# Performance work log

Measured on AMD Instinct MI355X. Metric: run time of the kernel, lower is better.

The kernel has to match this reference:

```python
import jax, jax.numpy as jnp
import numpy as np

N, E, F, H, C = 50000, 800000, 128, 128, 64
NEG_SLOPE = 0.2


def setup_inputs() -> dict:
    key = jax.random.key(0)
    ks = jax.random.split(key, 12)
    s = 1.0 / np.sqrt(H)
    return {
        "x": jax.random.normal(ks[0], (N, F), jnp.float32),
        "edge_index": jax.random.randint(ks[1], (2, E), 0, N, jnp.int64),
        "W1": jax.random.normal(ks[2], (F, H), jnp.float32) * s,
        "b1": jnp.zeros((H,), jnp.float32),
        "Wg1": jax.random.normal(ks[3], (H, H), jnp.float32) * s,
        "asrc1": jax.random.normal(ks[4], (H,), jnp.float32) * s,
        "adst1": jax.random.normal(ks[5], (H,), jnp.float32) * s,
        "bg1": jnp.zeros((H,), jnp.float32),
        "W2": jax.random.normal(ks[6], (H, H), jnp.float32) * s,
        "b2": jnp.zeros((H,), jnp.float32),
        "Wg2": jax.random.normal(ks[7], (H, H), jnp.float32) * s,
        "asrc2": jax.random.normal(ks[8], (H,), jnp.float32) * s,
        "adst2": jax.random.normal(ks[9], (H,), jnp.float32) * s,
        "bg2": jnp.zeros((H,), jnp.float32),
        "Wo": jax.random.normal(ks[10], (H, C), jnp.float32) * s,
        "bo": jnp.zeros((C,), jnp.float32),
    }


def _gcn(x, src, dst, n, W, b):
    # PyG GCNConv: add self-loops (done by caller), symmetric normalization
    xw = x @ W
    deg = jax.ops.segment_sum(jnp.ones(src.shape[0], xw.dtype), dst, num_segments=n)
    inv = jax.lax.rsqrt(deg)  # deg >= 1 due to self-loops
    coef = inv[src] * inv[dst]
    return jax.ops.segment_sum(coef[:, None] * xw[src], dst, num_segments=n) + b


def _gat(x, src, dst, n, W, a_s, a_d, b):
    # PyG GATConv, heads=1: segment softmax over destination nodes
    xw = x @ W
    e = jax.nn.leaky_relu((xw @ a_s)[src] + (xw @ a_d)[dst], NEG_SLOPE)
    m = jax.ops.segment_max(e, dst, num_segments=n)
    ex = jnp.exp(e - m[dst])
    denom = jax.ops.segment_sum(ex, dst, num_segments=n)
    alpha = ex / denom[dst]
    return jax.ops.segment_sum(alpha[:, None] * xw[src], dst, num_segments=n) + b


def reference(x, edge_index, W1, b1, Wg1, asrc1, adst1, bg1,
              W2, b2, Wg2, asrc2, adst2, bg2, Wo, bo):
    n = x.shape[0]
    loops = jnp.arange(n, dtype=edge_index.dtype)
    src = jnp.concatenate([edge_index[0], loops])
    dst = jnp.concatenate([edge_index[1], loops])

    h = jax.nn.relu(_gcn(x, src, dst, n, W1, b1))
    h = jax.nn.relu(_gat(h, src, dst, n, Wg1, asrc1, adst1, bg1))
    h = jax.nn.relu(_gcn(h, src, dst, n, W2, b2))
    h = jax.nn.relu(_gat(h, src, dst, n, Wg2, asrc2, adst2, bg2))
    z = h @ Wo + bo
    return (h, z)
```

## Files before the change

kernel.cpp:

```cpp
#include <hip/hip_runtime.h>
#include <hip/hip_bf16.h>
#include <hip/hip_fp16.h>


#define WAVE 64
#define BK 256
#define CHUNK 4096
#define NSLICE 4

typedef _Float16 f16x8 __attribute__((ext_vector_type(8)));
typedef float f32x4 __attribute__((ext_vector_type(4)));

__global__ void k_zero_i32(int* __restrict__ p, int n) {
    int i = blockIdx.x * 256 + threadIdx.x;
    if (i < n) p[i] = 0;
}


__global__ __launch_bounds__(256) void k_bhist(
    const int* __restrict__ ei, int* __restrict__ bcnt,
    int E, int Et, int nbuck) {
    __shared__ int hist[256];
    int tid = threadIdx.x;
    if (tid < nbuck) hist[tid] = 0;
    __syncthreads();
    for (int e = blockIdx.x * 256 + tid; e < Et; e += gridDim.x * 256) {
        int d = (e < E) ? ei[E + e] : (e - E);
        atomicAdd(&hist[d >> 8], 1);
    }
    __syncthreads();
    if (tid < nbuck && hist[tid] > 0) atomicAdd(&bcnt[tid], hist[tid]);
}

__global__ void k_bscan(const int* __restrict__ bcnt, int* __restrict__ bbase,
                        int* __restrict__ bcur, int nbuck) {
    __shared__ int tmp[256];
    int tid = threadIdx.x;
    int v = (tid < nbuck) ? bcnt[tid] : 0;
    tmp[tid] = v;
    __syncthreads();
    for (int off = 1; off < 256; off <<= 1) {
        int t = (tid >= off) ? tmp[tid - off] : 0;
        __syncthreads();
        tmp[tid] += t;
        __syncthreads();
    }
    if (tid < nbuck) {
        int excl = tmp[tid] - v;
        bbase[tid] = excl;
        bcur[tid] = excl;
        if (tid == nbuck - 1) bbase[nbuck] = tmp[tid];
    }
}

__global__ __launch_bounds__(256) void k_bscatter(
    const int* __restrict__ ei, int* __restrict__ bcur,
    int2* __restrict__ ebuf, int E, int Et, int nbuck) {
    __shared__ int hist[256];
    __shared__ int base[256];
    __shared__ int off[256];
    constexpr int PT = CHUNK / 256;
    int tid = threadIdx.x;
    int cb = blockIdx.x * CHUNK;
    if (tid < nbuck) { hist[tid] = 0; off[tid] = 0; }
    __syncthreads();

    int sv[PT], dv[PT];
#pragma unroll
    for (int i = 0; i < PT; ++i) {
        int e = cb + i * 256 + tid;
        int s = 0, d = -1;
        if (e < Et) {
            if (e < E) { s = ei[e]; d = ei[E + e]; }
            else       { s = d = e - E; }
            atomicAdd(&hist[d >> 8], 1);
        }
        sv[i] = s; dv[i] = d;
    }
    __syncthreads();
    if (tid < nbuck && hist[tid] > 0)
        base[tid] = atomicAdd(&bcur[tid], hist[tid]);
    __syncthreads();
#pragma unroll
    for (int i = 0; i < PT; ++i) {
        if (dv[i] >= 0) {
            int b = dv[i] >> 8;
            int pos = base[b] + atomicAdd(&off[b], 1);
            ebuf[pos] = make_int2(sv[i], dv[i]);
        }
    }
}

__global__ __launch_bounds__(256) void k_csr(
    const int2* __restrict__ ebuf, const int* __restrict__ bbase,
    int* __restrict__ rowp, float* __restrict__ inv, int* __restrict__ esrc,
    int Nn, int Et) {
    __shared__ int hist[256];
    __shared__ int scan[256];
    __shared__ int cur[256];
    int tid = threadIdx.x;
    int b = blockIdx.x;
    int bb = bbase[b], cnt = bbase[b + 1] - bb;
    hist[tid] = 0;
    __syncthreads();
    for (int t = tid; t < cnt; t += 256)
        atomicAdd(&hist[ebuf[bb + t].y & 255], 1);
    __syncthreads();
    int v = hist[tid];
    scan[tid] = v;
    __syncthreads();
    for (int o = 1; o < 256; o <<= 1) {
        int t = (tid >= o) ? scan[tid - o] : 0;
        __syncthreads();
        scan[tid] += t;
        __syncthreads();
    }
    int excl = scan[tid] - v;
    int node = b * BK + tid;
    if (node < Nn) {
        rowp[node] = bb + excl;
        inv[node] = rsqrtf((float)v);
    }
    cur[tid] = excl;
    if (b == 0 && tid == 0) rowp[Nn] = Et;
    __syncthreads();
    for (int t = tid; t < cnt; t += 256) {
        int2 e = ebuf[bb + t];
        int pos = bb + atomicAdd(&cur[e.y & 255], 1);
        esrc[pos] = e.x;
    }
}


__global__ void k_wcvt(const float* __restrict__ W1, const float* __restrict__ Wg1,
                       const float* __restrict__ W2, const float* __restrict__ Wg2,
                       const float* __restrict__ Wo, __half* __restrict__ Wt) {
    int i = blockIdx.x * 256 + threadIdx.x;
    if (i < 65536) {
        int w = i >> 14;
        int j = i & 16383;
        int nt = j >> 11, ks = (j >> 9) & 3, lane = (j >> 3) & 63, jj = j & 7;
        int n = nt * 16 + (lane & 15);
        int k = ks * 32 + (lane >> 4) * 8 + jj;
        const float* W = (w == 0) ? W1 : (w == 1) ? Wg1 : (w == 2) ? W2 : Wg2;
        Wt[i] = __float2half(W[k * 128 + n]);
    } else if (i < 73728) {
        int j = i - 65536;
        int nt = j >> 11, ks = (j >> 9) & 3, lane = (j >> 3) & 63, jj = j & 7;
        int n = nt * 16 + (lane & 15);
        int k = ks * 32 + (lane >> 4) * 8 + jj;
        Wt[65536 + j] = __float2half(Wo[k * 64 + n]);
    }
}


template <int NC, typename OT>
__global__ __launch_bounds__(256) void gemm_mfma(
    const float* __restrict__ A, const __half* __restrict__ Wt,
    const float* __restrict__ bias, OT* __restrict__ out,
    const float* __restrict__ asrc, const float* __restrict__ adst,
    float* __restrict__ alS, float* __restrict__ alD, int M) {
    constexpr int NT = NC / 16;
    __shared__ f16x8 Wl[NC * 16];
    const int tid = threadIdx.x;
    const int wv = tid >> 6, lane = tid & 63;
    const int m16 = lane & 15, quad = lane >> 4;

#pragma unroll
    for (int i = tid; i < NC * 16; i += 256)
        Wl[i] = ((const f16x8*)Wt)[i];
    __syncthreads();

    const int row0 = blockIdx.x * 64 + wv * 16;

    f16x8 af[4];
    {
        int row = row0 + m16;
        if (row > M - 1) row = M - 1;
        const float* ap = A + (size_t)row * 128 + quad * 8;
#pragma unroll
        for (int ks = 0; ks < 4; ++ks) {
            float4 lo = *(const float4*)(ap + ks * 32);
            float4 hi = *(const float4*)(ap + ks * 32 + 4);
            f16x8 v;
            v[0] = (_Float16)lo.x; v[1] = (_Float16)lo.y;
            v[2] = (_Float16)lo.z; v[3] = (_Float16)lo.w;
            v[4] = (_Float16)hi.x; v[5] = (_Float16)hi.y;
            v[6] = (_Float16)hi.z; v[7] = (_Float16)hi.w;
            af[ks] = v;
        }
    }

    f32x4 acc[NT];
#pragma unroll
    for (int nt = 0; nt < NT; ++nt)
        acc[nt] = (f32x4){0.f, 0.f, 0.f, 0.f};

#pragma unroll
    for (int ks = 0; ks < 4; ++ks) {
#pragma unroll
        for (int nt = 0; nt < NT; ++nt) {
            f16x8 bf = Wl[(nt * 4 + ks) * 64 + lane];
            acc[nt] = __builtin_amdgcn_mfma_f32_16x16x32_f16(
                af[ks], bf, acc[nt], 0, 0, 0);
        }
    }

    if (asrc) {
        float sa[NT], da[NT];
#pragma unroll
        for (int nt = 0; nt < NT; ++nt) {
            sa[nt] = asrc[nt * 16 + m16];
            da[nt] = adst[nt * 16 + m16];
        }
#pragma unroll
        for (int r = 0; r < 4; ++r) {
            float s = 0.f, d = 0.f;
#pragma unroll
            for (int nt = 0; nt < NT; ++nt) {
                s = fmaf(acc[nt][r], sa[nt], s);
                d = fmaf(acc[nt][r], da[nt], d);
            }
#pragma unroll
            for (int off = 8; off > 0; off >>= 1) {
                s += __shfl_xor(s, off);
                d += __shfl_xor(d, off);
            }
            int row = row0 + quad * 4 + r;
            if (m16 == 0 && row < M) { alS[row] = s; alD[row] = d; }
        }
    }

#pragma unroll
    for (int nt = 0; nt < NT; ++nt) {
#pragma unroll
        for (int r = 0; r < 4; ++r) {
            int row = row0 + quad * 4 + r;
            if (row < M) {
                float v = acc[nt][r];
                int col = nt * 16 + m16;
                if constexpr (sizeof(OT) == 2) {
                    size_t addr = ((size_t)(col >> 5) * M + row) * 32 + (col & 31);
                    ((__half*)out)[addr] = __float2half(v);
                } else {
                    ((float*)out)[(size_t)row * NC + col] = v + bias[col];
                }
            }
        }
    }
}


__global__ __launch_bounds__(256) void k_wgcn(
    const int* __restrict__ rowp, const int* __restrict__ esrc,
    const float* __restrict__ inv, int2* __restrict__ ew, int Nn) {
    int gid = blockIdx.x * 256 + threadIdx.x;
    int n = gid >> 6, lane = gid & 63;
    if (n >= Nn) return;
    int beg = rowp[n], end = rowp[n + 1];
    float invd = inv[n];
    for (int e = beg + lane; e < end; e += WAVE) {
        int sid = esrc[e];
        ew[e] = make_int2(sid, __float_as_int(invd * inv[sid]));
    }
}

__global__ __launch_bounds__(256) void k_alpha(
    const int* __restrict__ rowp, const int* __restrict__ esrc,
    const float* __restrict__ as_, const float* __restrict__ ad_,
    int2* __restrict__ ew, int Nn) {
    int gid = blockIdx.x * 256 + threadIdx.x;
    int n = gid >> 6, lane = gid & 63;
    if (n >= Nn) return;
    int beg = rowp[n], end = rowp[n + 1];
    int deg = end - beg;
    float adn = ad_[n];

    if (deg <= WAVE) {
        bool valid = (lane < deg);
        int sid = 0;
        float v = -1e30f;
        if (valid) {
            sid = esrc[beg + lane];
            float t = as_[sid] + adn;
            v = (t > 0.f) ? t : 0.2f * t;
        }
        float m = v;
#pragma unroll
        for (int off = 32; off > 0; off >>= 1) m = fmaxf(m, __shfl_xor(m, off));
        float ex = valid ? __expf(v - m) : 0.f;
        float ssum = ex;
#pragma unroll
        for (int off = 32; off > 0; off >>= 1) ssum += __shfl_xor(ssum, off);
        float wgt = ex * (1.f / ssum);
        if (valid) ew[beg + lane] = make_int2(sid, __float_as_int(wgt));
    } else {
        float m = -1e30f, ssum = 0.f;
        for (int e = beg + lane; e < end; e += WAVE) {
            float v = as_[esrc[e]] + adn;
            v = (v > 0.f) ? v : 0.2f * v;
            float mn = fmaxf(m, v);
            ssum = ssum * __expf(m - mn) + __expf(v - mn);
            m = mn;
        }
#pragma unroll
        for (int off = 32; off > 0; off >>= 1) {
            float mo = __shfl_xor(m, off);
            float so = __shfl_xor(ssum, off);
            float mn = fmaxf(m, mo);
            ssum = ssum * __expf(m - mn) + so * __expf(mo - mn);
            m = mn;
        }
        float rden = 1.f / ssum;
        for (int e = beg + lane; e < end; e += WAVE) {
            int sid = esrc[e];
            float v = as_[sid] + adn;
            v = (v > 0.f) ? v : 0.2f * v;
            ew[e] = make_int2(sid, __float_as_int(__expf(v - m) * rden));
        }
    }
}


__device__ __forceinline__ void acc8(float acc[8], float4 v, float w) {
    const __half2* h2 = (const __half2*)&v;
#pragma unroll
    for (int i = 0; i < 4; ++i) {
        float2 f = __half22float2(h2[i]);
        acc[2 * i]     = fmaf(w, f.x, acc[2 * i]);
        acc[2 * i + 1] = fmaf(w, f.y, acc[2 * i + 1]);
    }
}

__global__ __launch_bounds__(256) void k_agg(
    const __half* __restrict__ xw2, const int* __restrict__ rowp,
    const int2* __restrict__ ew, const float* __restrict__ bias,
    float* __restrict__ out, int Nn) {
    int tid = threadIdx.x;
    int slice = blockIdx.x & 3;
    int nb = blockIdx.x >> 2;
    int wv = tid >> 6, lane = tid & 63;
    int n = nb * 64 + wv * 16 + (lane >> 2);
    int q = lane & 3;
    if (n >= Nn) return;
    int beg = rowp[n], end = rowp[n + 1];
    const __half* xs = xw2 + (size_t)slice * Nn * 32 + q * 8;

    float acc[8] = {0.f, 0.f, 0.f, 0.f, 0.f, 0.f, 0.f, 0.f};
    int e = beg;
    for (; e + 4 <= end; e += 4) {
        int2 p0 = ew[e], p1 = ew[e + 1], p2 = ew[e + 2], p3 = ew[e + 3];
        float4 v0 = *(const float4*)(xs + (size_t)p0.x * 32);
        float4 v1 = *(const float4*)(xs + (size_t)p1.x * 32);
        float4 v2 = *(const float4*)(xs + (size_t)p2.x * 32);
        float4 v3 = *(const float4*)(xs + (size_t)p3.x * 32);
        acc8(acc, v0, __int_as_float(p0.y));
        acc8(acc, v1, __int_as_float(p1.y));
        acc8(acc, v2, __int_as_float(p2.y));
        acc8(acc, v3, __int_as_float(p3.y));
    }
    for (; e < end; ++e) {
        int2 p = ew[e];
        float4 v = *(const float4*)(xs + (size_t)p.x * 32);
        acc8(acc, v, __int_as_float(p.y));
    }

    const float* bp = bias + slice * 32 + q * 8;
    float4 b0 = *(const float4*)(bp);
    float4 b1 = *(const float4*)(bp + 4);
    float4 r0, r1;
    r0.x = fmaxf(acc[0] + b0.x, 0.f);
    r0.y = fmaxf(acc[1] + b0.y, 0.f);
    r0.z = fmaxf(acc[2] + b0.z, 0.f);
    r0.w = fmaxf(acc[3] + b0.w, 0.f);
    r1.x = fmaxf(acc[4] + b1.x, 0.f);
    r1.y = fmaxf(acc[5] + b1.y, 0.f);
    r1.z = fmaxf(acc[6] + b1.z, 0.f);
    r1.w = fmaxf(acc[7] + b1.w, 0.f);
    float4* o = (float4*)(out + (size_t)n * 128 + slice * 32 + q * 8);
    o[0] = r0;
    o[1] = r1;
}


extern "C" void kernel_launch(void* const* d_in, const int* in_sizes, int n_in,
                              void* d_out, int out_size, void* d_ws, size_t ws_size,
                              hipStream_t stream) {
    const float* x   = (const float*)d_in[0];
    const int*   ei  = (const int*)d_in[1];
    const float* W1  = (const float*)d_in[2];
    const float* b1  = (const float*)d_in[3];
    const float* Wg1 = (const float*)d_in[4];
    const float* as1 = (const float*)d_in[5];
    const float* ad1 = (const float*)d_in[6];
    const float* bg1 = (const float*)d_in[7];
    const float* W2  = (const float*)d_in[8];
    const float* b2  = (const float*)d_in[9];
    const float* Wg2 = (const float*)d_in[10];
    const float* as2 = (const float*)d_in[11];
    const float* ad2 = (const float*)d_in[12];
    const float* bg2 = (const float*)d_in[13];
    const float* Wo  = (const float*)d_in[14];
    const float* bo  = (const float*)d_in[15];

    const int Nn = in_sizes[0] / 128;
    const int E  = in_sizes[1] / 2;
    const int Et = E + Nn;
    const int H  = 128;
    const int nbuck = (Nn + BK - 1) / BK;

    float* outH = (float*)d_out;
    float* outZ = outH + (size_t)Nn * H;

    char* p = (char*)d_ws;
    auto carve = [&](size_t bytes) {
        char* r = p;
        p += (bytes + 255) & ~(size_t)255;
        return r;
    };
    __half* bufA = (__half*)carve((size_t)Nn * H * sizeof(__half));
    __half* Wt   = (__half*)carve((size_t)73728 * sizeof(__half));
    float* alS   = (float*)carve((size_t)Nn * sizeof(float));
    float* alD   = (float*)carve((size_t)Nn * sizeof(float));
    float* inv   = (float*)carve((size_t)Nn * sizeof(float));
    int*   rowp  = (int*)carve((size_t)(Nn + 1) * sizeof(int));
    int*   esrc  = (int*)carve((size_t)Et * sizeof(int));
    int2*  ebuf  = (int2*)carve((size_t)Et * sizeof(int2));
    int2*  ewg   = (int2*)carve((size_t)Et * sizeof(int2));
    int*   bcnt  = (int*)carve((size_t)nbuck * sizeof(int));
    int*   bbase = (int*)carve((size_t)(nbuck + 1) * sizeof(int));
    int*   bcur  = (int*)carve((size_t)nbuck * sizeof(int));
    (void)ws_size; (void)n_in; (void)out_size;

    int2* ewa = ebuf;

    const int nodeWaves = (Nn * WAVE + 255) / 256;
    const int gemmB = (Nn + 63) / 64;
    const int aggB  = ((Nn + 63) / 64) * NSLICE;
    const int scatB = (Et + CHUNK - 1) / CHUNK;

    k_zero_i32<<<1, 256, 0, stream>>>(bcnt, nbuck);
    k_bhist<<<104, 256, 0, stream>>>(ei, bcnt, E, Et, nbuck);
    k_bscan<<<1, 256, 0, stream>>>(bcnt, bbase, bcur, nbuck);
    k_bscatter<<<scatB, 256, 0, stream>>>(ei, bcur, ebuf, E, Et, nbuck);
    k_csr<<<nbuck, 256, 0, stream>>>(ebuf, bbase, rowp, inv, esrc, Nn, Et);
    k_wcvt<<<288, 256, 0, stream>>>(W1, Wg1, W2, Wg2, Wo, Wt);
    k_wgcn<<<nodeWaves, 256, 0, stream>>>(rowp, esrc, inv, ewg, Nn);

    gemm_mfma<128, __half><<<gemmB, 256, 0, stream>>>(
        x, Wt, nullptr, bufA, nullptr, nullptr, nullptr, nullptr, Nn);
    k_agg<<<aggB, 256, 0, stream>>>(bufA, rowp, ewg, b1, outH, Nn);

    gemm_mfma<128, __half><<<gemmB, 256, 0, stream>>>(
        outH, Wt + 16384, nullptr, bufA, as1, ad1, alS, alD, Nn);
    k_alpha<<<nodeWaves, 256, 0, stream>>>(rowp, esrc, alS, alD, ewa, Nn);
    k_agg<<<aggB, 256, 0, stream>>>(bufA, rowp, ewa, bg1, outH, Nn);

    gemm_mfma<128, __half><<<gemmB, 256, 0, stream>>>(
        outH, Wt + 32768, nullptr, bufA, nullptr, nullptr, nullptr, nullptr, Nn);
    k_agg<<<aggB, 256, 0, stream>>>(bufA, rowp, ewg, b2, outH, Nn);

    gemm_mfma<128, __half><<<gemmB, 256, 0, stream>>>(
        outH, Wt + 49152, nullptr, bufA, as2, ad2, alS, alD, Nn);
    k_alpha<<<nodeWaves, 256, 0, stream>>>(rowp, esrc, alS, alD, ewa, Nn);
    k_agg<<<aggB, 256, 0, stream>>>(bufA, rowp, ewa, bg2, outH, Nn);

    gemm_mfma<64, float><<<gemmB, 256, 0, stream>>>(
        outH, Wt + 65536, bo, outZ, nullptr, nullptr, nullptr, nullptr, Nn);
}
```

Before: 382.0 us.

## Slice features by XCC with persistent work-stealing aggregation and fp16 intermediates

Aggregation is rewritten as a persistent kernel that splits features into 8 slices of 16 columns. Each XCC starts on its own slice and grabs node chunks through atomic cursors, so a slice's gathered rows stay in that die's cache. Intermediate hidden layers are now stored as sliced fp16 and fed straight into the next GEMM instead of fp32 rows, halving that traffic. The histogram and weight-convert kernels are merged and the zeroing kernel becomes a memset. The costs are dynamic scheduling overhead, an extra buffer, and fp16 rounding of the hidden activations.

```diff
diff --git a/kernel.cpp b/kernel.cpp
--- a/kernel.cpp
+++ b/kernel.cpp
@@ -6,20 +6,19 @@
 #define WAVE 64
 #define BK 256
 #define CHUNK 4096
-#define NSLICE 4
+#define NSL 8
+#define CURSTRIDE 16
+#define NCHUNK 128
 
 typedef _Float16 f16x8 __attribute__((ext_vector_type(8)));
 typedef float f32x4 __attribute__((ext_vector_type(4)));
 
-__global__ void k_zero_i32(int* __restrict__ p, int n) {
-    int i = blockIdx.x * 256 + threadIdx.x;
-    if (i < n) p[i] = 0;
-}
-
-
-__global__ __launch_bounds__(256) void k_bhist(
-    const int* __restrict__ ei, int* __restrict__ bcnt,
-    int E, int Et, int nbuck) {
+
+__global__ __launch_bounds__(256) void k_bhist_wcvt(
+    const int* __restrict__ ei, int* __restrict__ bcnt, int E, int Et, int nbuck,
+    const float* __restrict__ W1, const float* __restrict__ Wg1,
+    const float* __restrict__ W2, const float* __restrict__ Wg2,
+    const float* __restrict__ Wo, __half* __restrict__ Wt) {
     __shared__ int hist[256];
     int tid = threadIdx.x;
     if (tid < nbuck) hist[tid] = 0;
@@ -30,112 +29,8 @@
     }
     __syncthreads();
     if (tid < nbuck && hist[tid] > 0) atomicAdd(&bcnt[tid], hist[tid]);
-}
-
-__global__ void k_bscan(const int* __restrict__ bcnt, int* __restrict__ bbase,
-                        int* __restrict__ bcur, int nbuck) {
-    __shared__ int tmp[256];
-    int tid = threadIdx.x;
-    int v = (tid < nbuck) ? bcnt[tid] : 0;
-    tmp[tid] = v;
-    __syncthreads();
-    for (int off = 1; off < 256; off <<= 1) {
-        int t = (tid >= off) ? tmp[tid - off] : 0;
-        __syncthreads();
-        tmp[tid] += t;
-        __syncthreads();
-    }
-    if (tid < nbuck) {
-        int excl = tmp[tid] - v;
-        bbase[tid] = excl;
-        bcur[tid] = excl;
-        if (tid == nbuck - 1) bbase[nbuck] = tmp[tid];
-    }
-}
-
-__global__ __launch_bounds__(256) void k_bscatter(
-    const int* __restrict__ ei, int* __restrict__ bcur,
-    int2* __restrict__ ebuf, int E, int Et, int nbuck) {
-    __shared__ int hist[256];
-    __shared__ int base[256];
-    __shared__ int off[256];
-    constexpr int PT = CHUNK / 256;
-    int tid = threadIdx.x;
-    int cb = blockIdx.x * CHUNK;
-    if (tid < nbuck) { hist[tid] = 0; off[tid] = 0; }
-    __syncthreads();
-
-    int sv[PT], dv[PT];
-#pragma unroll
-    for (int i = 0; i < PT; ++i) {
-        int e = cb + i * 256 + tid;
-        int s = 0, d = -1;
-        if (e < Et) {
-            if (e < E) { s = ei[e]; d = ei[E + e]; }
-            else       { s = d = e - E; }
-            atomicAdd(&hist[d >> 8], 1);
-        }
-        sv[i] = s; dv[i] = d;
-    }
-    __syncthreads();
-    if (tid < nbuck && hist[tid] > 0)
-        base[tid] = atomicAdd(&bcur[tid], hist[tid]);
-    __syncthreads();
-#pragma unroll
-    for (int i = 0; i < PT; ++i) {
-        if (dv[i] >= 0) {
-            int b = dv[i] >> 8;
-            int pos = base[b] + atomicAdd(&off[b], 1);
-            ebuf[pos] = make_int2(sv[i], dv[i]);
-        }
-    }
-}
-
-__global__ __launch_bounds__(256) void k_csr(
-    const int2* __restrict__ ebuf, const int* __restrict__ bbase,
-    int* __restrict__ rowp, float* __restrict__ inv, int* __restrict__ esrc,
-    int Nn, int Et) {
-    __shared__ int hist[256];
-    __shared__ int scan[256];
-    __shared__ int cur[256];
-    int tid = threadIdx.x;
-    int b = blockIdx.x;
-    int bb = bbase[b], cnt = bbase[b + 1] - bb;
-    hist[tid] = 0;
-    __syncthreads();
-    for (int t = tid; t < cnt; t += 256)
-        atomicAdd(&hist[ebuf[bb + t].y & 255], 1);
-    __syncthreads();
-    int v = hist[tid];
-    scan[tid] = v;
-    __syncthreads();
-    for (int o = 1; o < 256; o <<= 1) {
-        int t = (tid >= o) ? scan[tid - o] : 0;
-        __syncthreads();
-        scan[tid] += t;
-        __syncthreads();
-    }
-    int excl = scan[tid] - v;
-    int node = b * BK + tid;
-    if (node < Nn) {
-        rowp[node] = bb + excl;
-        inv[node] = rsqrtf((float)v);
-    }
-    cur[tid] = excl;
-    if (b == 0 && tid == 0) rowp[Nn] = Et;
-    __syncthreads();
-    for (int t = tid; t < cnt; t += 256) {
-        int2 e = ebuf[bb + t];
-        int pos = bb + atomicAdd(&cur[e.y & 255], 1);
-        esrc[pos] = e.x;
-    }
-}
-
-
-__global__ void k_wcvt(const float* __restrict__ W1, const float* __restrict__ Wg1,
-                       const float* __restrict__ W2, const float* __restrict__ Wg2,
-                       const float* __restrict__ Wo, __half* __restrict__ Wt) {
-    int i = blockIdx.x * 256 + threadIdx.x;
+
+    int i = blockIdx.x * 256 + tid;
     if (i < 65536) {
         int w = i >> 14;
         int j = i & 16383;
@@ -153,100 +48,102 @@
     }
 }
 
-
-template <int NC, typename OT>
-__global__ __launch_bounds__(256) void gemm_mfma(
-    const float* __restrict__ A, const __half* __restrict__ Wt,
-    const float* __restrict__ bias, OT* __restrict__ out,
-    const float* __restrict__ asrc, const float* __restrict__ adst,
-    float* __restrict__ alS, float* __restrict__ alD, int M) {
-    constexpr int NT = NC / 16;
-    __shared__ f16x8 Wl[NC * 16];
-    const int tid = threadIdx.x;
-    const int wv = tid >> 6, lane = tid & 63;
-    const int m16 = lane & 15, quad = lane >> 4;
-
-#pragma unroll
-    for (int i = tid; i < NC * 16; i += 256)
-        Wl[i] = ((const f16x8*)Wt)[i];
-    __syncthreads();
-
-    const int row0 = blockIdx.x * 64 + wv * 16;
-
-    f16x8 af[4];
-    {
-        int row = row0 + m16;
-        if (row > M - 1) row = M - 1;
-        const float* ap = A + (size_t)row * 128 + quad * 8;
-#pragma unroll
-        for (int ks = 0; ks < 4; ++ks) {
-            float4 lo = *(const float4*)(ap + ks * 32);
-            float4 hi = *(const float4*)(ap + ks * 32 + 4);
-            f16x8 v;
-            v[0] = (_Float16)lo.x; v[1] = (_Float16)lo.y;
-            v[2] = (_Float16)lo.z; v[3] = (_Float16)lo.w;
-            v[4] = (_Float16)hi.x; v[5] = (_Float16)hi.y;
-            v[6] = (_Float16)hi.z; v[7] = (_Float16)hi.w;
-            af[ks] = v;
-        }
-    }
-
-    f32x4 acc[NT];
-#pragma unroll
-    for (int nt = 0; nt < NT; ++nt)
-        acc[nt] = (f32x4){0.f, 0.f, 0.f, 0.f};
-
-#pragma unroll
-    for (int ks = 0; ks < 4; ++ks) {
-#pragma unroll
-        for (int nt = 0; nt < NT; ++nt) {
-            f16x8 bf = Wl[(nt * 4 + ks) * 64 + lane];
-            acc[nt] = __builtin_amdgcn_mfma_f32_16x16x32_f16(
-                af[ks], bf, acc[nt], 0, 0, 0);
-        }
-    }
-
-    if (asrc) {
-        float sa[NT], da[NT];
-#pragma unroll
-        for (int nt = 0; nt < NT; ++nt) {
-            sa[nt] = asrc[nt * 16 + m16];
-            da[nt] = adst[nt * 16 + m16];
-        }
-#pragma unroll
-        for (int r = 0; r < 4; ++r) {
-            float s = 0.f, d = 0.f;
-#pragma unroll
-            for (int nt = 0; nt < NT; ++nt) {
-                s = fmaf(acc[nt][r], sa[nt], s);
-                d = fmaf(acc[nt][r], da[nt], d);
-            }
-#pragma unroll
-            for (int off = 8; off > 0; off >>= 1) {
-                s += __shfl_xor(s, off);
-                d += __shfl_xor(d, off);
-            }
-            int row = row0 + quad * 4 + r;
-            if (m16 == 0 && row < M) { alS[row] = s; alD[row] = d; }
-        }
-    }
-
-#pragma unroll
-    for (int nt = 0; nt < NT; ++nt) {
-#pragma unroll
-        for (int r = 0; r < 4; ++r) {
-            int row = row0 + quad * 4 + r;
-            if (row < M) {
-                float v = acc[nt][r];
-                int col = nt * 16 + m16;
-                if constexpr (sizeof(OT) == 2) {
-                    size_t addr = ((size_t)(col >> 5) * M + row) * 32 + (col & 31);
-                    ((__half*)out)[addr] = __float2half(v);
-                } else {
-                    ((float*)out)[(size_t)row * NC + col] = v + bias[col];
-                }
-            }
-        }
+__global__ void k_bscan(const int* __restrict__ bcnt, int* __restrict__ bbase,
+                        int* __restrict__ bcur, int nbuck) {
+    __shared__ int tmp[256];
+    int tid = threadIdx.x;
+    int v = (tid < nbuck) ? bcnt[tid] : 0;
+    tmp[tid] = v;
+    __syncthreads();
+    for (int off = 1; off < 256; off <<= 1) {
+        int t = (tid >= off) ? tmp[tid - off] : 0;
+        __syncthreads();
+        tmp[tid] += t;
+        __syncthreads();
+    }
+    if (tid < nbuck) {
+        int excl = tmp[tid] - v;
+        bbase[tid] = excl;
+        bcur[tid] = excl;
+        if (tid == nbuck - 1) bbase[nbuck] = tmp[tid];
+    }
+}
+
+__global__ __launch_bounds__(256) void k_bscatter(
+    const int* __restrict__ ei, int* __restrict__ bcur,
+    int2* __restrict__ ebuf, int E, int Et, int nbuck) {
+    __shared__ int hist[256];
+    __shared__ int base[256];
+    __shared__ int off[256];
+    constexpr int PT = CHUNK / 256;
+    int tid = threadIdx.x;
+    int cb = blockIdx.x * CHUNK;
+    if (tid < nbuck) { hist[tid] = 0; off[tid] = 0; }
+    __syncthreads();
+
+    int sv[PT], dv[PT];
+#pragma unroll
+    for (int i = 0; i < PT; ++i) {
+        int e = cb + i * 256 + tid;
+        int s = 0, d = -1;
+        if (e < Et) {
+            if (e < E) { s = ei[e]; d = ei[E + e]; }
+            else       { s = d = e - E; }
+            atomicAdd(&hist[d >> 8], 1);
+        }
+        sv[i] = s; dv[i] = d;
+    }
+    __syncthreads();
+    if (tid < nbuck && hist[tid] > 0)
+        base[tid] = atomicAdd(&bcur[tid], hist[tid]);
+    __syncthreads();
+#pragma unroll
+    for (int i = 0; i < PT; ++i) {
+        if (dv[i] >= 0) {
+            int b = dv[i] >> 8;
+            int pos = base[b] + atomicAdd(&off[b], 1);
+            ebuf[pos] = make_int2(sv[i], dv[i]);
+        }
+    }
+}
+
+__global__ __launch_bounds__(256) void k_csr(
+    const int2* __restrict__ ebuf, const int* __restrict__ bbase,
+    int* __restrict__ rowp, float* __restrict__ inv, int* __restrict__ esrc,
+    int Nn, int Et) {
+    __shared__ int hist[256];
+    __shared__ int scan[256];
+    __shared__ int cur[256];
+    int tid = threadIdx.x;
+    int b = blockIdx.x;
+    int bb = bbase[b], cnt = bbase[b + 1] - bb;
+    hist[tid] = 0;
+    __syncthreads();
+    for (int t = tid; t < cnt; t += 256)
+        atomicAdd(&hist[ebuf[bb + t].y & 255], 1);
+    __syncthreads();
+    int v = hist[tid];
+    scan[tid] = v;
+    __syncthreads();
+    for (int o = 1; o < 256; o <<= 1) {
+        int t = (tid >= o) ? scan[tid - o] : 0;
+        __syncthreads();
+        scan[tid] += t;
+        __syncthreads();
+    }
+    int excl = scan[tid] - v;
+    int node = b * BK + tid;
+    if (node < Nn) {
+        rowp[node] = bb + excl;
+        inv[node] = rsqrtf((float)v);
+    }
+    cur[tid] = excl;
+    if (b == 0 && tid == 0) rowp[Nn] = Et;
+    __syncthreads();
+    for (int t = tid; t < cnt; t += 256) {
+        int2 e = ebuf[bb + t];
+        int pos = bb + atomicAdd(&cur[e.y & 255], 1);
+        esrc[pos] = e.x;
     }
 }
 
@@ -322,64 +219,195 @@
 }
 
 
-__device__ __forceinline__ void acc8(float acc[8], float4 v, float w) {
-    const __half2* h2 = (const __half2*)&v;
-#pragma unroll
-    for (int i = 0; i < 4; ++i) {
-        float2 f = __half22float2(h2[i]);
-        acc[2 * i]     = fmaf(w, f.x, acc[2 * i]);
-        acc[2 * i + 1] = fmaf(w, f.y, acc[2 * i + 1]);
-    }
-}
-
-__global__ __launch_bounds__(256) void k_agg(
-    const __half* __restrict__ xw2, const int* __restrict__ rowp,
+template <typename AT, bool ASLICE, int NC, typename OT>
+__global__ __launch_bounds__(256) void gemm_mfma(
+    const AT* __restrict__ A, const __half* __restrict__ Wt,
+    const float* __restrict__ bias, OT* __restrict__ out,
+    const float* __restrict__ asrc, const float* __restrict__ adst,
+    float* __restrict__ alS, float* __restrict__ alD, int M) {
+    constexpr int NT = NC / 16;
+    __shared__ f16x8 Wl[NC * 16];
+    const int tid = threadIdx.x;
+    const int wv = tid >> 6, lane = tid & 63;
+    const int m16 = lane & 15, quad = lane >> 4;
+
+#pragma unroll
+    for (int i = tid; i < NC * 16; i += 256)
+        Wl[i] = ((const f16x8*)Wt)[i];
+    __syncthreads();
+
+    const int row0 = blockIdx.x * 64 + wv * 16;
+
+    f16x8 af[4];
+    {
+        int row = row0 + m16;
+        if (row > M - 1) row = M - 1;
+        if constexpr (ASLICE) {
+            const __half* ab = (const __half*)A;
+#pragma unroll
+            for (int ks = 0; ks < 4; ++ks) {
+                int sl = ks * 2 + (quad >> 1);
+                af[ks] = *(const f16x8*)(ab + ((size_t)sl * M + row) * 16
+                                         + (quad & 1) * 8);
+            }
+        } else {
+            const float* ap = (const float*)A + (size_t)row * 128 + quad * 8;
+#pragma unroll
+            for (int ks = 0; ks < 4; ++ks) {
+                float4 lo = *(const float4*)(ap + ks * 32);
+                float4 hi = *(const float4*)(ap + ks * 32 + 4);
+                f16x8 v;
+                v[0] = (_Float16)lo.x; v[1] = (_Float16)lo.y;
+                v[2] = (_Float16)lo.z; v[3] = (_Float16)lo.w;
+                v[4] = (_Float16)hi.x; v[5] = (_Float16)hi.y;
+                v[6] = (_Float16)hi.z; v[7] = (_Float16)hi.w;
+                af[ks] = v;
+            }
+        }
+    }
+
+    f32x4 acc[NT];
+#pragma unroll
+    for (int nt = 0; nt < NT; ++nt)
+        acc[nt] = (f32x4){0.f, 0.f, 0.f, 0.f};
+
+#pragma unroll
+    for (int ks = 0; ks < 4; ++ks) {
+#pragma unroll
+        for (int nt = 0; nt < NT; ++nt) {
+            f16x8 bf = Wl[(nt * 4 + ks) * 64 + lane];
+            acc[nt] = __builtin_amdgcn_mfma_f32_16x16x32_f16(
+                af[ks], bf, acc[nt], 0, 0, 0);
+        }
+    }
+
+    if (asrc) {
+        float sa[NT], da[NT];
+#pragma unroll
+        for (int nt = 0; nt < NT; ++nt) {
+            sa[nt] = asrc[nt * 16 + m16];
+            da[nt] = adst[nt * 16 + m16];
+        }
+#pragma unroll
+        for (int r = 0; r < 4; ++r) {
+            float s = 0.f, d = 0.f;
+#pragma unroll
+            for (int nt = 0; nt < NT; ++nt) {
+                s = fmaf(acc[nt][r], sa[nt], s);
+                d = fmaf(acc[nt][r], da[nt], d);
+            }
+#pragma unroll
+            for (int off = 8; off > 0; off >>= 1) {
+                s += __shfl_xor(s, off);
+                d += __shfl_xor(d, off);
+            }
+            int row = row0 + quad * 4 + r;
+            if (m16 == 0 && row < M) { alS[row] = s; alD[row] = d; }
+        }
+    }
+
+#pragma unroll
+    for (int nt = 0; nt < NT; ++nt) {
+#pragma unroll
+        for (int r = 0; r < 4; ++r) {
+            int row = row0 + quad * 4 + r;
+            if (row < M) {
+                float v = acc[nt][r];
+                if constexpr (sizeof(OT) == 2) {
+                    ((__half*)out)[((size_t)nt * M + row) * 16 + m16] =
+                        __float2half(v);
+                } else {
+                    int col = nt * 16 + m16;
+                    ((float*)out)[(size_t)row * NC + col] = v + bias[col];
+                }
+            }
+        }
+    }
+}
+
+
+template <typename OT>
+__global__ __launch_bounds__(256) void k_agg_slice(
+    const __half* __restrict__ xs, const int* __restrict__ rowp,
     const int2* __restrict__ ew, const float* __restrict__ bias,
-    float* __restrict__ out, int Nn) {
-    int tid = threadIdx.x;
-    int slice = blockIdx.x & 3;
-    int nb = blockIdx.x >> 2;
-    int wv = tid >> 6, lane = tid & 63;
-    int n = nb * 64 + wv * 16 + (lane >> 2);
-    int q = lane & 3;
-    if (n >= Nn) return;
-    int beg = rowp[n], end = rowp[n + 1];
-    const __half* xs = xw2 + (size_t)slice * Nn * 32 + q * 8;
-
-    float acc[8] = {0.f, 0.f, 0.f, 0.f, 0.f, 0.f, 0.f, 0.f};
-    int e = beg;
-    for (; e + 4 <= end; e += 4) {
-        int2 p0 = ew[e], p1 = ew[e + 1], p2 = ew[e + 2], p3 = ew[e + 3];
-        float4 v0 = *(const float4*)(xs + (size_t)p0.x * 32);
-        float4 v1 = *(const float4*)(xs + (size_t)p1.x * 32);
-        float4 v2 = *(const float4*)(xs + (size_t)p2.x * 32);
-        float4 v3 = *(const float4*)(xs + (size_t)p3.x * 32);
-        acc8(acc, v0, __int_as_float(p0.y));
-        acc8(acc, v1, __int_as_float(p1.y));
-        acc8(acc, v2, __int_as_float(p2.y));
-        acc8(acc, v3, __int_as_float(p3.y));
-    }
-    for (; e < end; ++e) {
-        int2 p = ew[e];
-        float4 v = *(const float4*)(xs + (size_t)p.x * 32);
-        acc8(acc, v, __int_as_float(p.y));
-    }
-
-    const float* bp = bias + slice * 32 + q * 8;
-    float4 b0 = *(const float4*)(bp);
-    float4 b1 = *(const float4*)(bp + 4);
-    float4 r0, r1;
-    r0.x = fmaxf(acc[0] + b0.x, 0.f);
-    r0.y = fmaxf(acc[1] + b0.y, 0.f);
-    r0.z = fmaxf(acc[2] + b0.z, 0.f);
-    r0.w = fmaxf(acc[3] + b0.w, 0.f);
-    r1.x = fmaxf(acc[4] + b1.x, 0.f);
-    r1.y = fmaxf(acc[5] + b1.y, 0.f);
-    r1.z = fmaxf(acc[6] + b1.z, 0.f);
-    r1.w = fmaxf(acc[7] + b1.w, 0.f);
-    float4* o = (float4*)(out + (size_t)n * 128 + slice * 32 + q * 8);
-    o[0] = r0;
-    o[1] = r1;
+    OT* __restrict__ out, int* __restrict__ cursor, int Nn) {
+    __shared__ int chunk_sh;
+    int xcc;
+    asm volatile("s_getreg_b32 %0, hwreg(HW_REG_XCC_ID)" : "=s"(xcc));
+    xcc &= 7;
+    const int tid = threadIdx.x;
+    const int wv = tid >> 6, lane = tid & 63;
+    const int j = lane >> 1, half = lane & 1;
+
+    for (int pass = 0; pass < NSL; ++pass) {
+        const int slice = (xcc + pass) & (NSL - 1);
+        int* curp = cursor + slice * CURSTRIDE;
+        const __half* xsl = xs + (size_t)slice * Nn * 16 + half * 8;
+        float b8[8];
+        *(float4*)(b8)     = *(const float4*)(bias + slice * 16 + half * 8);
+        *(float4*)(b8 + 4) = *(const float4*)(bias + slice * 16 + half * 8 + 4);
+
+        for (;;) {
+            if (tid == 0) {
+                int c = *(volatile int*)curp;
+                chunk_sh = (c >= Nn) ? Nn : atomicAdd(curp, NCHUNK);
+            }
+            __syncthreads();
+            const int n0 = chunk_sh;
+            __syncthreads();
+            if (n0 >= Nn) break;
+            const int n = n0 + wv * 32 + j;
+            if (n < Nn) {
+                int beg = rowp[n], end = rowp[n + 1];
+                float acc[8] = {0.f,0.f,0.f,0.f,0.f,0.f,0.f,0.f};
+                int e = beg;
+                for (; e + 2 <= end; e += 2) {
+                    int2 p0 = ew[e];
+                    int2 p1 = ew[e + 1];
+                    f16x8 v0 = *(const f16x8*)(xsl + (size_t)p0.x * 16);
+                    f16x8 v1 = *(const f16x8*)(xsl + (size_t)p1.x * 16);
+                    float w0 = __int_as_float(p0.y);
+                    float w1 = __int_as_float(p1.y);
+#pragma unroll
+                    for (int i = 0; i < 8; ++i)
+                        acc[i] = fmaf(w0, (float)v0[i], acc[i]);
+#pragma unroll
+                    for (int i = 0; i < 8; ++i)
+                        acc[i] = fmaf(w1, (float)v1[i], acc[i]);
+                }
+                if (e < end) {
+                    int2 p = ew[e];
+                    f16x8 v = *(const f16x8*)(xsl + (size_t)p.x * 16);
+                    float w = __int_as_float(p.y);
+#pragma unroll
+                    for (int i = 0; i < 8; ++i)
+                        acc[i] = fmaf(w, (float)v[i], acc[i]);
+                }
+                if constexpr (sizeof(OT) == 2) {
+                    f16x8 hv;
+#pragma unroll
+                    for (int i = 0; i < 8; ++i)
+                        hv[i] = (_Float16)fmaxf(acc[i] + b8[i], 0.f);
+                    *(f16x8*)((__half*)out + ((size_t)slice * Nn + n) * 16
+                              + half * 8) = hv;
+                } else {
+                    float* op = (float*)out + (size_t)n * 128 + slice * 16
+                                + half * 8;
+                    float4 r0, r1;
+                    r0.x = fmaxf(acc[0] + b8[0], 0.f);
+                    r0.y = fmaxf(acc[1] + b8[1], 0.f);
+                    r0.z = fmaxf(acc[2] + b8[2], 0.f);
+                    r0.w = fmaxf(acc[3] + b8[3], 0.f);
+                    r1.x = fmaxf(acc[4] + b8[4], 0.f);
+                    r1.y = fmaxf(acc[5] + b8[5], 0.f);
+                    r1.z = fmaxf(acc[6] + b8[6], 0.f);
+                    r1.w = fmaxf(acc[7] + b8[7], 0.f);
+                    *(float4*)op = r0;
+                    *(float4*)(op + 4) = r1;
+                }
+            }
+        }
+    }
 }
 
 
@@ -419,6 +447,7 @@
         return r;
     };
     __half* bufA = (__half*)carve((size_t)Nn * H * sizeof(__half));
+    __half* bufB = (__half*)carve((size_t)Nn * H * sizeof(__half));
     __half* Wt   = (__half*)carve((size_t)73728 * sizeof(__half));
     float* alS   = (float*)carve((size_t)Nn * sizeof(float));
     float* alD   = (float*)carve((size_t)Nn * sizeof(float));
@@ -427,7 +456,10 @@
     int*   esrc  = (int*)carve((size_t)Et * sizeof(int));
     int2*  ebuf  = (int2*)carve((size_t)Et * sizeof(int2));
     int2*  ewg   = (int2*)carve((size_t)Et * sizeof(int2));
-    int*   bcnt  = (int*)carve((size_t)nbuck * sizeof(int));
+    const int nCurInts = 4 * NSL * CURSTRIDE;
+    int*   zreg  = (int*)carve((size_t)(nbuck + nCurInts) * sizeof(int));
+    int*   bcnt  = zreg;
+    int*   curs  = zreg + nbuck;
     int*   bbase = (int*)carve((size_t)(nbuck + 1) * sizeof(int));
     int*   bcur  = (int*)carve((size_t)nbuck * sizeof(int));
     (void)ws_size; (void)n_in; (void)out_size;
@@ -436,35 +468,39 @@
 
     const int nodeWaves = (Nn * WAVE + 255) / 256;
     const int gemmB = (Nn + 63) / 64;
-    const int aggB  = ((Nn + 63) / 64) * NSLICE;
     const int scatB = (Et + CHUNK - 1) / CHUNK;
-
-    k_zero_i32<<<1, 256, 0, stream>>>(bcnt, nbuck);
-    k_bhist<<<104, 256, 0, stream>>>(ei, bcnt, E, Et, nbuck);
+    const int aggB  = 1024;
+
+    hipMemsetAsync(zreg, 0, (size_t)(nbuck + nCurInts) * sizeof(int), stream);
+    k_bhist_wcvt<<<288, 256, 0, stream>>>(ei, bcnt, E, Et, nbuck,
+                                          W1, Wg1, W2, Wg2, Wo, Wt);
     k_bscan<<<1, 256, 0, stream>>>(bcnt, bbase, bcur, nbuck);
     k_bscatter<<<scatB, 256, 0, stream>>>(ei, bcur, ebuf, E, Et, nbuck);
     k_csr<<<nbuck, 256, 0, stream>>>(ebuf, bbase, rowp, inv, esrc, Nn, Et);
-    k_wcvt<<<288, 256, 0, stream>>>(W1, Wg1, W2, Wg2, Wo, Wt);
     k_wgcn<<<nodeWaves, 256, 0, stream>>>(rowp, esrc, inv, ewg, Nn);
 
-    gemm_mfma<128, __half><<<gemmB, 256, 0, stream>>>(
+    gemm_mfma<float, false, 128, __half><<<gemmB, 256, 0, stream>>>(
         x, Wt, nullptr, bufA, nullptr, nullptr, nullptr, nullptr, Nn);
-    k_agg<<<aggB, 256, 0, stream>>>(bufA, rowp, ewg, b1, outH, Nn);
-
-    gemm_mfma<128, __half><<<gemmB, 256, 0, stream>>>(
-        outH, Wt + 16384, nullptr, bufA, as1, ad1, alS, alD, Nn);
+    k_agg_slice<__half><<<aggB, 256, 0, stream>>>(
+        bufA, rowp, ewg, b1, bufB, curs + 0 * NSL * CURSTRIDE, Nn);
+
+    gemm_mfma<__half, true, 128, __half><<<gemmB, 256, 0, stream>>>(
+        bufB, Wt + 16384, nullptr, bufA, as1, ad1, alS, alD, Nn);
     k_alpha<<<nodeWaves, 256, 0, stream>>>(rowp, esrc, alS, alD, ewa, Nn);
-    k_agg<<<aggB, 256, 0, stream>>>(bufA, rowp, ewa, bg1, outH, Nn);
-
-    gemm_mfma<128, __half><<<gemmB, 256, 0, stream>>>(
-        outH, Wt + 32768, nullptr, bufA, nullptr, nullptr, nullptr, nullptr, Nn);
-    k_agg<<<aggB, 256, 0, stream>>>(bufA, rowp, ewg, b2, outH, Nn);
-
-    gemm_mfma<128, __half><<<gemmB, 256, 0, stream>>>(
-        outH, Wt + 49152, nullptr, bufA, as2, ad2, alS, alD, Nn);
+    k_agg_slice<__half><<<aggB, 256, 0, stream>>>(
+        bufA, rowp, ewa, bg1, bufB, curs + 1 * NSL * CURSTRIDE, Nn);
+
+    gemm_mfma<__half, true, 128, __half><<<gemmB, 256, 0, stream>>>(
+        bufB, Wt + 32768, nullptr, bufA, nullptr, nullptr, nullptr, nullptr, Nn);
+    k_agg_slice<__half><<<aggB, 256, 0, stream>>>(
+        bufA, rowp, ewg, b2, bufB, curs + 2 * NSL * CURSTRIDE, Nn);
+
+    gemm_mfma<__half, true, 128, __half><<<gemmB, 256, 0, stream>>>(
+        bufB, Wt + 49152, nullptr, bufA, as2, ad2, alS, alD, Nn);
     k_alpha<<<nodeWaves, 256, 0, stream>>>(rowp, esrc, alS, alD, ewa, Nn);
-    k_agg<<<aggB, 256, 0, stream>>>(bufA, rowp, ewa, bg2, outH, Nn);
-
-    gemm_mfma<64, float><<<gemmB, 256, 0, stream>>>(
+    k_agg_slice<float><<<aggB, 256, 0, stream>>>(
+        bufA, rowp, ewa, bg2, outH, curs + 3 * NSL * CURSTRIDE, Nn);
+
+    gemm_mfma<float, false, 64, float><<<gemmB, 256, 0, stream>>>(
         outH, Wt + 65536, bo, outZ, nullptr, nullptr, nullptr, nullptr, Nn);
 }
```

Measured after the change: 662.4 us. 73.4% more time.
